# Performance work log

Hardware: AMD Instinct MI355X
Metric: run time of the kernel (lower is better)

## Reference

```python
import jax, jax.numpy as jnp
import numpy as np

N, C, H, W = 2, 128, 64, 64
N_HEAD = 4
GROUPS = 16
EPS = 1e-5


def group_norm(x, scale, offset):
    # haiku GroupNorm, channels_first: normalize over (channels-in-group, h, w)
    n, c, h, w = x.shape
    xg = x.reshape(n, GROUPS, c // GROUPS, h, w)
    mu = xg.mean(axis=(2, 3, 4), keepdims=True)
    var = xg.var(axis=(2, 3, 4), keepdims=True)
    xg = (xg - mu) * jax.lax.rsqrt(var + EPS)
    return xg.reshape(n, c, h, w) * scale[None, :, None, None] + offset[None, :, None, None]


def setup_inputs() -> dict:
    key = jax.random.key(0)
    ks = jax.random.split(key, 4)
    inv_sqrt_c = 1.0 / np.sqrt(C).astype(np.float32)
    return {
        "x": jax.random.normal(ks[0], (N, C, H, W), dtype=jnp.float32),
        "w_qkv": jax.random.normal(ks[1], (C, 3 * C), dtype=jnp.float32) * inv_sqrt_c,
        "b_qkv": jnp.zeros((3 * C,), dtype=jnp.float32),
        "w_out": jax.random.normal(ks[2], (C, C), dtype=jnp.float32) * inv_sqrt_c,
        "b_out": jnp.zeros((C,), dtype=jnp.float32),
        "gn1_scale": jnp.ones((C,), dtype=jnp.float32),
        "gn1_offset": jnp.zeros((C,), dtype=jnp.float32),
        "gn2_scale": jnp.ones((C,), dtype=jnp.float32),
        "gn2_offset": jnp.zeros((C,), dtype=jnp.float32),
    }


def reference(x, w_qkv, b_qkv, w_out, b_out, gn1_scale, gn1_offset, gn2_scale, gn2_offset):
    n, c, h, w = x.shape
    dh = c // N_HEAD
    # GroupNorm (x is reassigned, so the residual uses the normalized x)
    xn = group_norm(x, gn1_scale, gn1_offset)
    # 1x1 conv qkv projection: [n, 3c, h, w]
    qkv = jnp.einsum('nchw,cd->ndhw', xn, w_qkv) + b_qkv[None, :, None, None]
    # [n, 3H, dh, hw] -> [n, 3H, hw, dh]
    qkv = jnp.swapaxes(qkv.reshape(n, N_HEAD * 3, dh, h * w), 2, 3)
    q, k, v = jnp.split(qkv, 3, axis=1)  # each [n, H, hw, dh]
    scale = dh ** (-0.25)
    # [n, H, hw, hw] attention matrix (the memory-bound core)
    att = jax.nn.softmax((q * scale) @ (jnp.swapaxes(k, 2, 3) * scale), axis=3)
    y = jnp.swapaxes(att @ v, 2, 3).reshape(n, c, h, w)
    # 1x1 conv out projection + GroupNorm + residual
    out = jnp.einsum('nchw,cd->ndhw', y, w_out) + b_out[None, :, None, None]
    return xn + group_norm(out, gn2_scale, gn2_offset)
```

## Files before the change

kernel.cpp:

```cpp
#include <hip/hip_runtime.h>
#include <hip/hip_bf16.h>
#include <math.h>

constexpr int cHW   = 4096;
constexpr int cC    = 128;
constexpr int cNH   = 4;
constexpr int cDH   = 32;
constexpr float cEPS = 1e-5f;
constexpr float cQS = 0.2550347805f;
constexpr int SPLIT = 4;

typedef short bh8  __attribute__((ext_vector_type(8)));
typedef float f4   __attribute__((ext_vector_type(4)));
typedef float f16a __attribute__((ext_vector_type(16)));

static __device__ __forceinline__ unsigned short f2bf(float f) {
  union { __hip_bfloat16 h; unsigned short u; } cv;
  cv.h = __float2bfloat16(f);
  return cv.u;
}
static __device__ __forceinline__ unsigned pack2bf(float a, float b) {
  return (unsigned)f2bf(a) | ((unsigned)f2bf(b) << 16);
}
static __device__ __forceinline__ unsigned pack_trunc(float a, float b) {
  unsigned ua = __builtin_bit_cast(unsigned, a);
  unsigned ub = __builtin_bit_cast(unsigned, b);
  return (ua >> 16) | (ub & 0xffff0000u);
}
static __device__ __forceinline__ float bflo(unsigned pk) {
  return __builtin_bit_cast(float, pk << 16);
}
static __device__ __forceinline__ float bfhi(unsigned pk) {
  return __builtin_bit_cast(float, pk & 0xffff0000u);
}
static __device__ __forceinline__ void plswap(unsigned& a, unsigned& b) {
#if __has_builtin(__builtin_amdgcn_permlane32_swap)
  typedef int v2i __attribute__((ext_vector_type(2)));
  v2i r = __builtin_amdgcn_permlane32_swap((int)a, (int)b, false, false);
  a = (unsigned)r[0]; b = (unsigned)r[1];
#else
  asm("v_permlane32_swap_b32 %0, %1" : "+v"(a), "+v"(b));
#endif
}
static __device__ __forceinline__ bh8 mk8(unsigned a, unsigned b, unsigned c, unsigned d) {
  union { unsigned u[4]; bh8 v; } t;
  t.u[0] = a; t.u[1] = b; t.u[2] = c; t.u[3] = d;
  return t.v;
}

__device__ __forceinline__ void block_reduce2(float& a, float& b, float* sbuf) {
  #pragma unroll
  for (int off = 32; off > 0; off >>= 1) {
    a += __shfl_down(a, off, 64);
    b += __shfl_down(b, off, 64);
  }
  int wave = threadIdx.x >> 6;
  int lane = threadIdx.x & 63;
  if (lane == 0) { sbuf[wave] = a; sbuf[4 + wave] = b; }
  __syncthreads();
  if (threadIdx.x == 0) {
    sbuf[8] = sbuf[0] + sbuf[1] + sbuf[2] + sbuf[3];
    sbuf[9] = sbuf[4] + sbuf[5] + sbuf[6] + sbuf[7];
  }
  __syncthreads();
  a = sbuf[8];
  b = sbuf[9];
}

__global__ __launch_bounds__(256)
void prep(const float* __restrict__ x, float* __restrict__ part,
          const float* __restrict__ wq, const float* __restrict__ wo,
          unsigned short* __restrict__ wqT, unsigned short* __restrict__ woT,
          float* __restrict__ stats2) {
  __shared__ float lds[32 * 133];
  int L = threadIdx.x;
  if (blockIdx.x < 256) {
    int ng = blockIdx.x >> 3, sl = blockIdx.x & 7;
    const float4* s4 = (const float4*)x;
    float s = 0.f, s2 = 0.f;
    #pragma unroll
    for (int i = 0; i < 4; i++) {
      int idx = i * 256 + L;
      int c = idx >> 7, tt = idx & 127;
      float4 v = s4[(size_t)(ng * 8 + c) * 1024 + sl * 128 + tt];
      s  += v.x + v.y + v.z + v.w;
      s2 += v.x*v.x + v.y*v.y + v.z*v.z + v.w*v.w;
    }
    block_reduce2(s, s2, lds);
    if (L == 0) { part[blockIdx.x * 2] = s; part[blockIdx.x * 2 + 1] = s2; }
  } else {
    int bx = blockIdx.x - 256;
    if (bx == 0 && L < 64) stats2[L] = 0.f;
    const float* src; unsigned short* dst; int W, d0;
    if (bx < 12) { src = wq; dst = wqT; W = 384; d0 = bx * 32; }
    else         { src = wo; dst = woT; W = 128; d0 = (bx - 12) * 32; }
    #pragma unroll
    for (int i = 0; i < 16; i++) {
      int c = i * 8 + (L >> 5), d = L & 31;
      lds[d * 133 + c] = src[(size_t)c * W + d0 + d];
    }
    __syncthreads();
    int d = L >> 3, ch = L & 7, c0 = ch * 16;
    unsigned pk[8];
    #pragma unroll
    for (int j = 0; j < 8; j++)
      pk[j] = pack2bf(lds[d * 133 + c0 + 2 * j], lds[d * 133 + c0 + 2 * j + 1]);
    uint4* d4 = (uint4*)(dst + (size_t)(d0 + d) * 128 + c0);
    d4[0] = make_uint4(pk[0], pk[1], pk[2], pk[3]);
    d4[1] = make_uint4(pk[4], pk[5], pk[6], pk[7]);
  }
}

__global__ __launch_bounds__(256)
void gn1_pack(const float* __restrict__ x, const float* __restrict__ part,
              const float* __restrict__ sc, const float* __restrict__ of,
              unsigned short* __restrict__ xnB) {
  int cc = blockIdx.x, ts = blockIdx.y, n = blockIdx.z;
  int ng = n * 16 + cc;
  float s = 0.f, s2 = 0.f;
  #pragma unroll
  for (int p = 0; p < 8; p++) { s += part[(ng*8+p)*2]; s2 += part[(ng*8+p)*2+1]; }
  float mu = s * (1.0f / 32768.0f);
  float rinv = rsqrtf(s2 * (1.0f / 32768.0f) - mu * mu + cEPS);
  int t = ts * 256 + threadIdx.x;
  float v[8];
  #pragma unroll
  for (int j = 0; j < 8; j++) {
    int c = cc * 8 + j;
    float a = rinv * sc[c];
    float bo = of[c] - mu * a;
    v[j] = x[((size_t)n * cC + c) * cHW + t] * a + bo;
  }
  unsigned pk[4];
  #pragma unroll
  for (int j = 0; j < 4; j++) pk[j] = pack2bf(v[2*j], v[2*j+1]);
  ((uint4*)xnB)[(size_t)(n * 16 + cc) * cHW + t] = make_uint4(pk[0], pk[1], pk[2], pk[3]);
}

__global__ __launch_bounds__(256)
void qkv_mfma(const unsigned short* __restrict__ xnB, const unsigned short* __restrict__ wqT,
              const float* __restrict__ bq, unsigned* __restrict__ qF,
              unsigned* __restrict__ kF, unsigned* __restrict__ vF) {
  __shared__ float vbuf[64 * 36];
  const int L = threadIdx.x & 63, w = threadIdx.x >> 6;
  const int c16 = L & 15, q = L >> 4;
  const int t0 = blockIdx.x * 64, dg = blockIdx.y, n = blockIdx.z;
  const int nh = n * 4 + (dg & 3), d0 = dg * 32;
  const f4 zf = {0.f, 0.f, 0.f, 0.f};
  f4 acc0 = zf, acc1 = zf;
  const int trow = t0 + w * 16 + c16;
  #pragma unroll
  for (int ks = 0; ks < 4; ks++) {
    bh8 a  = *(const bh8*)(xnB + ((size_t)(n * 16 + ks * 4 + q) * cHW + trow) * 8);
    bh8 b0 = *(const bh8*)(wqT + (size_t)(d0 + c16) * 128 + ks * 32 + q * 8);
    bh8 b1 = *(const bh8*)(wqT + (size_t)(d0 + 16 + c16) * 128 + ks * 32 + q * 8);
    acc0 = __builtin_amdgcn_mfma_f32_16x16x32_bf16(a, b0, acc0, 0, 0, 0);
    acc1 = __builtin_amdgcn_mfma_f32_16x16x32_bf16(a, b1, acc1, 0, 0, 0);
  }
  const float blo = bq[d0 + c16], bhi = bq[d0 + 16 + c16];
  const float scl = (dg < 4) ? cQS : 1.0f;
  #pragma unroll
  for (int r = 0; r < 4; r++) {
    vbuf[(w * 16 + q * 4 + r) * 36 + c16]      = (acc0[r] + blo) * scl;
    vbuf[(w * 16 + q * 4 + r) * 36 + 16 + c16] = (acc1[r] + bhi) * scl;
  }
  __syncthreads();
  const int tl = threadIdx.x >> 7, fr = (threadIdx.x >> 6) & 1, LL = threadIdx.x & 63;
  const int col = LL & 31, h2 = LL >> 5;
  unsigned pk[4];
  if (dg < 8) {
    const float* src = &vbuf[(tl * 32 + col) * 36 + fr * 16 + h2 * 8];
    #pragma unroll
    for (int jj = 0; jj < 4; jj++) pk[jj] = pack2bf(src[2 * jj], src[2 * jj + 1]);
  } else {
    const float* src = &vbuf[(tl * 32 + fr * 16 + h2 * 8) * 36 + col];
    #pragma unroll
    for (int jj = 0; jj < 4; jj++) pk[jj] = pack2bf(src[2 * jj * 36], src[(2 * jj + 1) * 36]);
  }
  unsigned* dst = (dg < 4) ? qF : ((dg < 8) ? kF : vF);
  size_t frag = ((size_t)(nh * 128 + (t0 >> 5) + tl) * 2 + fr) * 64 + LL;
  ((uint4*)dst)[frag] = make_uint4(pk[0], pk[1], pk[2], pk[3]);
}

__global__ __launch_bounds__(256, 4)
void flash_mfma(const unsigned short* __restrict__ qF,
                const unsigned short* __restrict__ kF,
                const unsigned short* __restrict__ vF,
                unsigned* __restrict__ opart, float* __restrict__ lpart) {
  const int w = threadIdx.x >> 6, L = threadIdx.x & 63;
  const int col = L & 31, hi = L >> 5;
  const int qt = blockIdx.x * 4 + w, nh = blockIdx.y, ph = blockIdx.z;
  const short oneb = 0x3F80;
  const bh8 ones = {oneb, oneb, oneb, oneb, oneb, oneb, oneb, oneb};
  const f16a zf16 = {0.f,0.f,0.f,0.f, 0.f,0.f,0.f,0.f, 0.f,0.f,0.f,0.f, 0.f,0.f,0.f,0.f};

  const unsigned short* qb = qF + ((size_t)(nh * 128 + qt) * 2) * 512;
  bh8 qf0 = *(const bh8*)(qb + L * 8);
  bh8 qf1 = *(const bh8*)(qb + 512 + L * 8);

  const unsigned short* kb = kF + (size_t)nh * 128 * 1024;
  const unsigned short* vb = vF + (size_t)nh * 128 * 1024;

  f16a o = zf16, lacc = zf16;

  const int tb0 = ph * (cHW / SPLIT / 32);
  #pragma unroll 2
  for (int tl = tb0; tl < tb0 + (cHW / SPLIT / 32); ++tl) {
    const unsigned short* kp = kb + (size_t)tl * 1024;
    const unsigned short* vp = vb + (size_t)tl * 1024;
    bh8 ka0 = *(const bh8*)(kp + L * 8);
    bh8 ka1 = *(const bh8*)(kp + 512 + L * 8);
    bh8 vfa = *(const bh8*)(vp + L * 8);
    bh8 vfb = *(const bh8*)(vp + 512 + L * 8);
    f16a s = __builtin_amdgcn_mfma_f32_32x32x16_bf16(ka0, qf0, zf16, 0, 0, 0);
    s = __builtin_amdgcn_mfma_f32_32x32x16_bf16(ka1, qf1, s, 0, 0, 0);
    #pragma unroll
    for (int r = 0; r < 16; r++) s[r] = __builtin_amdgcn_exp2f(s[r]);
    unsigned pk0 = pack_trunc(s[0],  s[1]);
    unsigned pk1 = pack_trunc(s[2],  s[3]);
    unsigned pk2 = pack_trunc(s[4],  s[5]);
    unsigned pk3 = pack_trunc(s[6],  s[7]);
    unsigned pk4 = pack_trunc(s[8],  s[9]);
    unsigned pk5 = pack_trunc(s[10], s[11]);
    unsigned pk6 = pack_trunc(s[12], s[13]);
    unsigned pk7 = pack_trunc(s[14], s[15]);
    plswap(pk0, pk2); plswap(pk1, pk3);
    plswap(pk4, pk6); plswap(pk5, pk7);
    bh8 pf0 = mk8(pk0, pk1, pk2, pk3);
    bh8 pf1 = mk8(pk4, pk5, pk6, pk7);
    o    = __builtin_amdgcn_mfma_f32_32x32x16_bf16(pf0, vfa,  o,    0, 0, 0);
    lacc = __builtin_amdgcn_mfma_f32_32x32x16_bf16(pf0, ones, lacc, 0, 0, 0);
    o    = __builtin_amdgcn_mfma_f32_32x32x16_bf16(pf1, vfb,  o,    0, 0, 0);
    lacc = __builtin_amdgcn_mfma_f32_32x32x16_bf16(pf1, ones, lacc, 0, 0, 0);
  }

  const size_t base = (size_t)ph * 32768 + (size_t)nh * cHW + (size_t)qt * 32;
  #pragma unroll
  for (int k = 0; k < 8; k++) {
    const int rowlo = ((2 * k) & 3) + 8 * (k >> 1) + 4 * hi;
    opart[((base + rowlo) >> 1) * 32 + col] = pack_trunc(o[2 * k], o[2 * k + 1]);
  }
  if (col == 0) {
    #pragma unroll
    for (int r = 0; r < 16; r++)
      lpart[base + (r & 3) + 8 * (r >> 2) + 4 * hi] = lacc[r];
  }
}

__global__ __launch_bounds__(512)
void out_fused(const unsigned* __restrict__ opart, const float* __restrict__ lpart,
               const unsigned short* __restrict__ woT, const float* __restrict__ bo,
               float* __restrict__ proj, float* __restrict__ stats2) {
  __shared__ uint4 afbuf[1024];
  __shared__ float obuf[64 * 136];
  const int L = threadIdx.x & 63, w = threadIdx.x >> 6;
  const int c16 = L & 15, q = L >> 4;
  const int t0 = blockIdx.x * 64, n = blockIdx.y;
  const int rg = w >> 1;
  const int trow = t0 + rg * 16 + c16;
  const f4 zf = {0.f, 0.f, 0.f, 0.f};

  #pragma unroll
  for (int i = 0; i < 2; i++) {
    const int h = (w & 1) * 2 + i;
    const size_t grow = (size_t)(n * 4 + h) * cHW + trow;
    float l = 0.f;
    #pragma unroll
    for (int p = 0; p < SPLIT; p++) l += lpart[(size_t)p * 32768 + grow];
    const size_t rp = grow >> 1;
    const int par = c16 & 1;
    float e[8];
    #pragma unroll
    for (int j = 0; j < 8; j++) e[j] = 0.f;
    #pragma unroll
    for (int p = 0; p < SPLIT; p++) {
      const uint4* op = (const uint4*)(opart + ((size_t)p * 16384 + rp) * 32 + q * 8);
      uint4 v0 = op[0], v1 = op[1];
      unsigned uu[8] = {v0.x, v0.y, v0.z, v0.w, v1.x, v1.y, v1.z, v1.w};
      #pragma unroll
      for (int j = 0; j < 8; j++)
        e[j] += par ? bfhi(uu[j]) : bflo(uu[j]);
    }
    const float inv = 1.0f / l;
    unsigned pk[4];
    #pragma unroll
    for (int jj = 0; jj < 4; jj++)
      pk[jj] = pack2bf(e[2 * jj] * inv, e[2 * jj + 1] * inv);
    afbuf[(rg * 4 + h) * 64 + L] = make_uint4(pk[0], pk[1], pk[2], pk[3]);
  }
  __syncthreads();

  #pragma unroll
  for (int i = 0; i < 2; i++) {
    const int dg = (w & 1) * 2 + i;
    const int d0 = dg * 32;
    f4 acc0 = zf, acc1 = zf;
    #pragma unroll
    for (int h = 0; h < 4; h++) {
      bh8 a  = *(const bh8*)&afbuf[(rg * 4 + h) * 64 + L];
      bh8 b0 = *(const bh8*)(woT + (size_t)(d0 + c16) * 128 + h * 32 + q * 8);
      bh8 b1 = *(const bh8*)(woT + (size_t)(d0 + 16 + c16) * 128 + h * 32 + q * 8);
      acc0 = __builtin_amdgcn_mfma_f32_16x16x32_bf16(a, b0, acc0, 0, 0, 0);
      acc1 = __builtin_amdgcn_mfma_f32_16x16x32_bf16(a, b1, acc1, 0, 0, 0);
    }
    const float blo = bo[d0 + c16], bhi = bo[d0 + 16 + c16];
    #pragma unroll
    for (int r = 0; r < 4; r++) {
      obuf[(rg * 16 + q * 4 + r) * 136 + d0 + c16]      = acc0[r] + blo;
      obuf[(rg * 16 + q * 4 + r) * 136 + d0 + 16 + c16] = acc1[r] + bhi;
    }
  }
  __syncthreads();

  const int t16 = threadIdx.x & 15, dd = threadIdx.x >> 4;
  float s = 0.f, s2 = 0.f;
  #pragma unroll
  for (int jd = 0; jd < 4; jd++) {
    const int d = dd * 4 + jd;
    #pragma unroll
    for (int tc = 0; tc < 4; tc++) {
      float v = obuf[(tc * 16 + t16) * 136 + d];
      proj[((size_t)n * cC + d) * cHW + t0 + tc * 16 + t16] = v;
      s += v; s2 += v * v;
    }
  }
  #pragma unroll
  for (int off = 16; off > 0; off >>= 1) {
    s  += __shfl_down(s, off, 32);
    s2 += __shfl_down(s2, off, 32);
  }
  if ((threadIdx.x & 31) == 0) {
    const int g = threadIdx.x >> 5;
    atomicAdd(&stats2[n * 32 + g * 2],     s);
    atomicAdd(&stats2[n * 32 + g * 2 + 1], s2);
  }
}

__global__ __launch_bounds__(256)
void gn2_apply(const float* __restrict__ x, const float* __restrict__ proj,
               const float* __restrict__ p1, const float* __restrict__ p2,
               const float* __restrict__ s1, const float* __restrict__ o1,
               const float* __restrict__ s2, const float* __restrict__ o2,
               float* __restrict__ out) {
  int tid = blockIdx.x * 256 + threadIdx.x;
  int Cg = tid >> 8;
  int n = Cg >> 7, ch = Cg & 127, g = ch >> 3, ng = n * 16 + g;
  float sa = 0.f, sb = 0.f;
  #pragma unroll
  for (int p = 0; p < 8; p++) {
    sa += p1[(ng*8+p)*2]; sb += p1[(ng*8+p)*2+1];
  }
  float ta = p2[ng * 2], tb = p2[ng * 2 + 1];
  float mu1 = sa * (1.0f/32768.0f);
  float ri1 = rsqrtf(sb * (1.0f/32768.0f) - mu1*mu1 + cEPS);
  float a1 = ri1 * s1[ch], b1 = o1[ch] - mu1 * a1;
  float mu2 = ta * (1.0f/32768.0f);
  float ri2 = rsqrtf(tb * (1.0f/32768.0f) - mu2*mu2 + cEPS);
  float a2 = ri2 * s2[ch], b2 = o2[ch] - mu2 * a2;
  const float4* x4 = (const float4*)x;
  const float4* pr4 = (const float4*)proj;
  float4* o4 = (float4*)out;
  #pragma unroll
  for (int i = 0; i < 4; i++) {
    size_t f = (size_t)tid * 4 + i;
    float4 xv = x4[f], pv = pr4[f];
    float4 r;
    r.x = xv.x * a1 + b1 + pv.x * a2 + b2;
    r.y = xv.y * a1 + b1 + pv.y * a2 + b2;
    r.z = xv.z * a1 + b1 + pv.z * a2 + b2;
    r.w = xv.w * a1 + b1 + pv.w * a2 + b2;
    o4[f] = r;
  }
}

extern "C" void kernel_launch(void* const* d_in, const int* in_sizes, int n_in,
                              void* d_out, int out_size, void* d_ws, size_t ws_size,
                              hipStream_t stream) {
  const float* x     = (const float*)d_in[0];
  const float* w_qkv = (const float*)d_in[1];
  const float* b_qkv = (const float*)d_in[2];
  const float* w_out = (const float*)d_in[3];
  const float* b_out = (const float*)d_in[4];
  const float* g1s   = (const float*)d_in[5];
  const float* g1o   = (const float*)d_in[6];
  const float* g2s   = (const float*)d_in[7];
  const float* g2o   = (const float*)d_in[8];
  float* out = (float*)d_out;
  float* ws  = (float*)d_ws;

  const size_t MAP = (size_t)2 * cC * cHW;
  float* proj    = ws;
  float* lpart   = proj + MAP;
  float* stats1  = lpart + (size_t)SPLIT * 32768;
  float* stats2  = stats1 + 512;
  unsigned* opart = (unsigned*)(stats2 + 512);
  unsigned* qF   = opart + (size_t)SPLIT * 32768 * 16;
  unsigned* kF   = qF + MAP / 2;
  unsigned* vF   = kF + MAP / 2;
  unsigned short* xnB = (unsigned short*)(vF + MAP / 2);
  unsigned short* wqT = xnB + MAP;
  unsigned short* woT = wqT + 49152;

  prep      <<<dim3(272),           256, 0, stream>>>(x, stats1, w_qkv, w_out, wqT, woT,
                                                      stats2);
  gn1_pack  <<<dim3(16, 16, 2),     256, 0, stream>>>(x, stats1, g1s, g1o, xnB);
  qkv_mfma  <<<dim3(64, 12, 2),     256, 0, stream>>>(xnB, wqT, b_qkv, qF, kF, vF);
  flash_mfma<<<dim3(32, 8, SPLIT),  256, 0, stream>>>((const unsigned short*)qF,
                                                      (const unsigned short*)kF,
                                                      (const unsigned short*)vF,
                                                      opart, lpart);
  out_fused <<<dim3(64, 2),         512, 0, stream>>>(opart, lpart, woT, b_out,
                                                      proj, stats2);
  gn2_apply <<<dim3(256),           256, 0, stream>>>(x, proj, stats1, stats2,
                                                      g1s, g1o, g2s, g2o, out);
}
```

Measured before the change: 138.6 us.

## Split out-projection across channel blocks and replace GN2 atomics with partial sums

The out-projection kernel is re-gridded so each 256-thread block handles one 32-channel slice for 64 pixels, keeping the A fragments in registers instead of staging them through LDS. This gives four times more blocks. Group-norm-2 statistics are now written as per-block partial sums and reduced inside gn2_apply, which removes the global atomics and the zeroing in prep. The flash kernel moves to 128-thread blocks with twice as many blocks. The cost is that each out block recomputes the normalized attention fragments for all heads, so that work is done four times.

After: 124.9 us. 9.8% less time.

```diff
diff --git a/kernel.cpp b/kernel.cpp
--- a/kernel.cpp
+++ b/kernel.cpp
@@ -70,8 +70,7 @@
 __global__ __launch_bounds__(256)
 void prep(const float* __restrict__ x, float* __restrict__ part,
           const float* __restrict__ wq, const float* __restrict__ wo,
-          unsigned short* __restrict__ wqT, unsigned short* __restrict__ woT,
-          float* __restrict__ stats2) {
+          unsigned short* __restrict__ wqT, unsigned short* __restrict__ woT) {
   __shared__ float lds[32 * 133];
   int L = threadIdx.x;
   if (blockIdx.x < 256) {
@@ -90,7 +89,6 @@
     if (L == 0) { part[blockIdx.x * 2] = s; part[blockIdx.x * 2 + 1] = s2; }
   } else {
     int bx = blockIdx.x - 256;
-    if (bx == 0 && L < 64) stats2[L] = 0.f;
     const float* src; unsigned short* dst; int W, d0;
     if (bx < 12) { src = wq; dst = wqT; W = 384; d0 = bx * 32; }
     else         { src = wo; dst = woT; W = 128; d0 = (bx - 12) * 32; }
@@ -182,14 +180,14 @@
   ((uint4*)dst)[frag] = make_uint4(pk[0], pk[1], pk[2], pk[3]);
 }
 
-__global__ __launch_bounds__(256, 4)
+__global__ __launch_bounds__(128, 4)
 void flash_mfma(const unsigned short* __restrict__ qF,
                 const unsigned short* __restrict__ kF,
                 const unsigned short* __restrict__ vF,
                 unsigned* __restrict__ opart, float* __restrict__ lpart) {
   const int w = threadIdx.x >> 6, L = threadIdx.x & 63;
   const int col = L & 31, hi = L >> 5;
-  const int qt = blockIdx.x * 4 + w, nh = blockIdx.y, ph = blockIdx.z;
+  const int qt = blockIdx.x * 2 + w, nh = blockIdx.y, ph = blockIdx.z;
   const short oneb = 0x3F80;
   const bh8 ones = {oneb, oneb, oneb, oneb, oneb, oneb, oneb, oneb};
   const f16a zf16 = {0.f,0.f,0.f,0.f, 0.f,0.f,0.f,0.f, 0.f,0.f,0.f,0.f, 0.f,0.f,0.f,0.f};
@@ -247,22 +245,20 @@
   }
 }
 
-__global__ __launch_bounds__(512)
+__global__ __launch_bounds__(256)
 void out_fused(const unsigned* __restrict__ opart, const float* __restrict__ lpart,
                const unsigned short* __restrict__ woT, const float* __restrict__ bo,
-               float* __restrict__ proj, float* __restrict__ stats2) {
-  __shared__ uint4 afbuf[1024];
-  __shared__ float obuf[64 * 136];
+               float* __restrict__ proj, float* __restrict__ part2) {
+  __shared__ float obuf[64 * 36];
   const int L = threadIdx.x & 63, w = threadIdx.x >> 6;
   const int c16 = L & 15, q = L >> 4;
-  const int t0 = blockIdx.x * 64, n = blockIdx.y;
-  const int rg = w >> 1;
-  const int trow = t0 + rg * 16 + c16;
+  const int t0 = blockIdx.x * 64, d0 = blockIdx.y * 32, n = blockIdx.z;
   const f4 zf = {0.f, 0.f, 0.f, 0.f};
-
-  #pragma unroll
-  for (int i = 0; i < 2; i++) {
-    const int h = (w & 1) * 2 + i;
+  const int trow = t0 + w * 16 + c16;
+
+  bh8 afrag[4];
+  #pragma unroll
+  for (int h = 0; h < 4; h++) {
     const size_t grow = (size_t)(n * 4 + h) * cHW + trow;
     float l = 0.f;
     #pragma unroll
@@ -286,53 +282,50 @@
     #pragma unroll
     for (int jj = 0; jj < 4; jj++)
       pk[jj] = pack2bf(e[2 * jj] * inv, e[2 * jj + 1] * inv);
-    afbuf[(rg * 4 + h) * 64 + L] = make_uint4(pk[0], pk[1], pk[2], pk[3]);
+    afrag[h] = mk8(pk[0], pk[1], pk[2], pk[3]);
+  }
+
+  f4 acc0 = zf, acc1 = zf;
+  #pragma unroll
+  for (int h = 0; h < 4; h++) {
+    bh8 b0 = *(const bh8*)(woT + (size_t)(d0 + c16) * 128 + h * 32 + q * 8);
+    bh8 b1 = *(const bh8*)(woT + (size_t)(d0 + 16 + c16) * 128 + h * 32 + q * 8);
+    acc0 = __builtin_amdgcn_mfma_f32_16x16x32_bf16(afrag[h], b0, acc0, 0, 0, 0);
+    acc1 = __builtin_amdgcn_mfma_f32_16x16x32_bf16(afrag[h], b1, acc1, 0, 0, 0);
+  }
+  float blo = bo[d0 + c16], bhi = bo[d0 + 16 + c16];
+  #pragma unroll
+  for (int r = 0; r < 4; r++) {
+    obuf[(w * 16 + q * 4 + r) * 36 + c16]      = acc0[r] + blo;
+    obuf[(w * 16 + q * 4 + r) * 36 + 16 + c16] = acc1[r] + bhi;
   }
   __syncthreads();
 
-  #pragma unroll
-  for (int i = 0; i < 2; i++) {
-    const int dg = (w & 1) * 2 + i;
-    const int d0 = dg * 32;
-    f4 acc0 = zf, acc1 = zf;
-    #pragma unroll
-    for (int h = 0; h < 4; h++) {
-      bh8 a  = *(const bh8*)&afbuf[(rg * 4 + h) * 64 + L];
-      bh8 b0 = *(const bh8*)(woT + (size_t)(d0 + c16) * 128 + h * 32 + q * 8);
-      bh8 b1 = *(const bh8*)(woT + (size_t)(d0 + 16 + c16) * 128 + h * 32 + q * 8);
-      acc0 = __builtin_amdgcn_mfma_f32_16x16x32_bf16(a, b0, acc0, 0, 0, 0);
-      acc1 = __builtin_amdgcn_mfma_f32_16x16x32_bf16(a, b1, acc1, 0, 0, 0);
-    }
-    const float blo = bo[d0 + c16], bhi = bo[d0 + 16 + c16];
-    #pragma unroll
-    for (int r = 0; r < 4; r++) {
-      obuf[(rg * 16 + q * 4 + r) * 136 + d0 + c16]      = acc0[r] + blo;
-      obuf[(rg * 16 + q * 4 + r) * 136 + d0 + 16 + c16] = acc1[r] + bhi;
-    }
-  }
-  __syncthreads();
-
-  const int t16 = threadIdx.x & 15, dd = threadIdx.x >> 4;
-  float s = 0.f, s2 = 0.f;
-  #pragma unroll
-  for (int jd = 0; jd < 4; jd++) {
-    const int d = dd * 4 + jd;
-    #pragma unroll
-    for (int tc = 0; tc < 4; tc++) {
-      float v = obuf[(tc * 16 + t16) * 136 + d];
-      proj[((size_t)n * cC + d) * cHW + t0 + tc * 16 + t16] = v;
-      s += v; s2 += v * v;
-    }
-  }
-  #pragma unroll
-  for (int off = 16; off > 0; off >>= 1) {
-    s  += __shfl_down(s, off, 32);
-    s2 += __shfl_down(s2, off, 32);
-  }
-  if ((threadIdx.x & 31) == 0) {
-    const int g = threadIdx.x >> 5;
-    atomicAdd(&stats2[n * 32 + g * 2],     s);
-    atomicAdd(&stats2[n * 32 + g * 2 + 1], s2);
+  int t16 = threadIdx.x & 15, d8 = (threadIdx.x >> 4) & 15;
+  float s[2] = {0.f, 0.f}, s2v[2] = {0.f, 0.f};
+  #pragma unroll
+  for (int tc = 0; tc < 4; tc++)
+    #pragma unroll
+    for (int hh = 0; hh < 2; hh++) {
+      int d = d8 + hh * 16;
+      float v = obuf[(tc * 16 + t16) * 36 + d];
+      proj[((size_t)n * cC + d0 + d) * cHW + t0 + tc * 16 + t16] = v;
+      s[hh] += v; s2v[hh] += v * v;
+    }
+  #pragma unroll
+  for (int hh = 0; hh < 2; hh++) {
+    float a = s[hh], b = s2v[hh];
+    #pragma unroll
+    for (int off = 32; off > 0; off >>= 1) {
+      a += __shfl_down(a, off, 64);
+      b += __shfl_down(b, off, 64);
+    }
+    if (L == 0) {
+      int g = (d0 + w * 4 + hh * 16) >> 3;
+      size_t idx = (((size_t)(n * 16 + g) * 128) + blockIdx.x * 2 + (w & 1)) * 2;
+      part2[idx]     = a;
+      part2[idx + 1] = b;
+    }
   }
 }
 
@@ -342,17 +335,30 @@
                const float* __restrict__ s1, const float* __restrict__ o1,
                const float* __restrict__ s2, const float* __restrict__ o2,
                float* __restrict__ out) {
+  __shared__ float sb[2];
   int tid = blockIdx.x * 256 + threadIdx.x;
-  int Cg = tid >> 8;
+  int Cg = blockIdx.x;
   int n = Cg >> 7, ch = Cg & 127, g = ch >> 3, ng = n * 16 + g;
-  float sa = 0.f, sb = 0.f;
+  if (threadIdx.x < 64) {
+    int sl = threadIdx.x;
+    float a = p2[((size_t)ng * 128 + sl) * 2]     + p2[((size_t)ng * 128 + 64 + sl) * 2];
+    float b = p2[((size_t)ng * 128 + sl) * 2 + 1] + p2[((size_t)ng * 128 + 64 + sl) * 2 + 1];
+    #pragma unroll
+    for (int off = 32; off > 0; off >>= 1) {
+      a += __shfl_down(a, off, 64);
+      b += __shfl_down(b, off, 64);
+    }
+    if (threadIdx.x == 0) { sb[0] = a; sb[1] = b; }
+  }
+  float sa = 0.f, sbv = 0.f;
   #pragma unroll
   for (int p = 0; p < 8; p++) {
-    sa += p1[(ng*8+p)*2]; sb += p1[(ng*8+p)*2+1];
-  }
-  float ta = p2[ng * 2], tb = p2[ng * 2 + 1];
+    sa += p1[(ng*8+p)*2]; sbv += p1[(ng*8+p)*2+1];
+  }
+  __syncthreads();
+  float ta = sb[0], tb = sb[1];
   float mu1 = sa * (1.0f/32768.0f);
-  float ri1 = rsqrtf(sb * (1.0f/32768.0f) - mu1*mu1 + cEPS);
+  float ri1 = rsqrtf(sbv * (1.0f/32768.0f) - mu1*mu1 + cEPS);
   float a1 = ri1 * s1[ch], b1 = o1[ch] - mu1 * a1;
   float mu2 = ta * (1.0f/32768.0f);
   float ri2 = rsqrtf(tb * (1.0f/32768.0f) - mu2*mu2 + cEPS);
@@ -392,8 +398,8 @@
   float* proj    = ws;
   float* lpart   = proj + MAP;
   float* stats1  = lpart + (size_t)SPLIT * 32768;
-  float* stats2  = stats1 + 512;
-  unsigned* opart = (unsigned*)(stats2 + 512);
+  float* part2   = stats1 + 512;
+  unsigned* opart = (unsigned*)(part2 + 8192);
   unsigned* qF   = opart + (size_t)SPLIT * 32768 * 16;
   unsigned* kF   = qF + MAP / 2;
   unsigned* vF   = kF + MAP / 2;
@@ -401,16 +407,15 @@
   unsigned short* wqT = xnB + MAP;
   unsigned short* woT = wqT + 49152;
 
-  prep      <<<dim3(272),           256, 0, stream>>>(x, stats1, w_qkv, w_out, wqT, woT,
-                                                      stats2);
+  prep      <<<dim3(272),           256, 0, stream>>>(x, stats1, w_qkv, w_out, wqT, woT);
   gn1_pack  <<<dim3(16, 16, 2),     256, 0, stream>>>(x, stats1, g1s, g1o, xnB);
   qkv_mfma  <<<dim3(64, 12, 2),     256, 0, stream>>>(xnB, wqT, b_qkv, qF, kF, vF);
-  flash_mfma<<<dim3(32, 8, SPLIT),  256, 0, stream>>>((const unsigned short*)qF,
+  flash_mfma<<<dim3(64, 8, SPLIT),  128, 0, stream>>>((const unsigned short*)qF,
                                                       (const unsigned short*)kF,
                                                       (const unsigned short*)vF,
                                                       opart, lpart);
-  out_fused <<<dim3(64, 2),         512, 0, stream>>>(opart, lpart, woT, b_out,
-                                                      proj, stats2);
-  gn2_apply <<<dim3(256),           256, 0, stream>>>(x, proj, stats1, stats2,
+  out_fused <<<dim3(64, 4, 2),      256, 0, stream>>>(opart, lpart, woT, b_out,
+                                                      proj, part2);
+  gn2_apply <<<dim3(256),           256, 0, stream>>>(x, proj, stats1, part2,
                                                       g1s, g1o, g2s, g2o, out);
 }
```
